# Performance work log

Measured on AMD Instinct MI355X. Metric: run time of the kernel, lower is better.

The kernel has to match this reference:

```python
import jax, jax.numpy as jnp
import numpy as np

N = 50000        # nodes
E = 800000       # edges (before self-loops)
F_IN = 128       # in_features
HID = 128        # hidden_size
HEADS = 4
NEG_SLOPE = 0.2  # PyG GATConv default


def setup_inputs() -> dict:
    key = jax.random.key(0)
    ks = jax.random.split(key, 16)
    def w(k, shape, fan_in):
        return jax.random.normal(k, shape, dtype=jnp.float32) / np.sqrt(fan_in)
    x = jax.random.normal(ks[0], (N, F_IN), dtype=jnp.float32)
    edge_index = jax.random.randint(ks[1], (2, E), 0, N, dtype=jnp.int64)
    return {
        "x": x,
        "edge_index": edge_index,
        # encoder: HEADS independent GATConv(F_IN -> HID, heads=1)
        "enc_W": w(ks[2], (HEADS, F_IN, HID), F_IN),
        "enc_asrc": w(ks[3], (HEADS, HID), HID),
        "enc_adst": w(ks[4], (HEADS, HID), HID),
        "enc_b": jnp.zeros((HEADS, HID), jnp.float32),
        "enc_lin_W": w(ks[5], (HEADS * HID, HID), HEADS * HID),
        "enc_lin_b": jnp.zeros((HID,), jnp.float32),
        # decoder: HEADS independent GATConv(HID -> F_IN, heads=1)
        "dec_W": w(ks[6], (HEADS, HID, F_IN), HID),
        "dec_asrc": w(ks[7], (HEADS, F_IN), F_IN),
        "dec_adst": w(ks[8], (HEADS, F_IN), F_IN),
        "dec_b": jnp.zeros((HEADS, F_IN), jnp.float32),
        "dec_lin_W": w(ks[9], (HEADS * F_IN, F_IN), HEADS * F_IN),
        "dec_lin_b": jnp.zeros((F_IN,), jnp.float32),
    }


def _gat_head(x, src, dst, W, a_src, a_dst, b, n):
    # PyG GATConv, heads=1: h = xW; e = leaky_relu(a_src.h_src + a_dst.h_dst)
    # alpha = segment-softmax over incoming edges of dst; out = scatter-add + b
    h = x @ W                                   # [n, out]
    e = (h @ a_src)[src] + (h @ a_dst)[dst]     # [Etot]
    e = jax.nn.leaky_relu(e, NEG_SLOPE)
    m = jax.ops.segment_max(e, dst, num_segments=n)
    ew = jnp.exp(e - m[dst])
    denom = jax.ops.segment_sum(ew, dst, num_segments=n)
    alpha = ew / denom[dst]                     # self-loops guarantee denom > 0
    out = jax.ops.segment_sum(alpha[:, None] * h[src], dst, num_segments=n)
    return out + b


def _multihead(x, src, dst, Ws, asrc, adst, bs, lin_W, lin_b, n):
    heads = [_gat_head(x, src, dst, Ws[h], asrc[h], adst[h], bs[h], n)
             for h in range(Ws.shape[0])]
    cat = jnp.concatenate(heads, axis=1)        # [n, heads*out]
    return jax.nn.relu(cat @ lin_W + lin_b)


def reference(x, edge_index, enc_W, enc_asrc, enc_adst, enc_b, enc_lin_W,
              enc_lin_b, dec_W, dec_asrc, dec_adst, dec_b, dec_lin_W,
              dec_lin_b):
    n = x.shape[0]
    loop = jnp.arange(n, dtype=edge_index.dtype)
    src = jnp.concatenate([edge_index[0], loop])  # add self-loops (PyG default)
    dst = jnp.concatenate([edge_index[1], loop])
    enc = _multihead(x, src, dst, enc_W, enc_asrc, enc_adst, enc_b,
                     enc_lin_W, enc_lin_b, n)
    dec = _multihead(enc, src, dst, dec_W, dec_asrc, dec_adst, dec_b,
                     dec_lin_W, dec_lin_b, n)
    return dec
```

## Files before the change

### kernel.cpp

```cpp
#include <hip/hip_runtime.h>
#include <hip/hip_fp16.h>
#include <cstdint>
#include <cstddef>


#define FDIM   128
#define HEADS  4
#define HCAT   512

typedef unsigned short u16;
typedef __attribute__((ext_vector_type(4))) float f32x4;
typedef __attribute__((ext_vector_type(8))) short bf16x8;

__device__ __forceinline__ u16 f2b_rne(float f) {
    unsigned u = __float_as_uint(f);
    unsigned r = (u + 0x7FFFu + ((u >> 16) & 1u)) >> 16;
    return (u16)r;
}
__device__ __forceinline__ float b2f(u16 h) {
    return __uint_as_float(((unsigned)h) << 16);
}

__global__ void k_detect(const void* ei, int E, int N, int* flag) {
    if (threadIdx.x == 0 && blockIdx.x == 0) {
        const long long* p = (const long long*)ei;
        int bad = 0;
        int n = E < 64 ? E : 64;
        for (int i = 0; i < n; ++i) {
            long long v = p[i];
            if (v < 0 || v >= (long long)N) bad = 1;
        }
        *flag = bad;
    }
}

__device__ __forceinline__ int edge_at(const void* ei, int is32, long long pos) {
    return is32 ? ((const int*)ei)[pos] : (int)(((const long long*)ei)[pos]);
}

__global__ void k_zero_i32(int* p, int n) {
    int i = blockIdx.x * blockDim.x + threadIdx.x;
    if (i < n) p[i] = 0;
}

__global__ void k_count(const void* ei, const int* flag, int E, int N, int* deg) {
    int e = blockIdx.x * blockDim.x + threadIdx.x;
    int Etot = E + N;
    if (e >= Etot) return;
    int is32 = *flag;
    int dst = (e < E) ? edge_at(ei, is32, (long long)E + e) : (e - E);
    atomicAdd(&deg[dst], 1);
}

#define SCAN_BLOCKS 256
#define SCAN_TPB    256

__global__ __launch_bounds__(SCAN_TPB) void k_scan1(const int* __restrict__ deg,
                                                    int* __restrict__ bsum, int N) {
    __shared__ int sdata[SCAN_TPB];
    int b = blockIdx.x;
    int chunk = (N + SCAN_BLOCKS - 1) / SCAN_BLOCKS;
    int start = b * chunk;
    int end = start + chunk;
    if (start > N) start = N;
    if (end > N) end = N;
    int s = 0;
    for (int i = start + threadIdx.x; i < end; i += SCAN_TPB) s += deg[i];
    sdata[threadIdx.x] = s;
    __syncthreads();
    for (int o = SCAN_TPB / 2; o; o >>= 1) {
        if (threadIdx.x < o) sdata[threadIdx.x] += sdata[threadIdx.x + o];
        __syncthreads();
    }
    if (threadIdx.x == 0) bsum[b] = sdata[0];
}

__global__ __launch_bounds__(SCAN_BLOCKS) void k_scan2(const int* __restrict__ bsum,
                                                       int* __restrict__ bbase,
                                                       int* __restrict__ off_last) {
    __shared__ int sdata[SCAN_BLOCKS];
    int t = threadIdx.x;
    sdata[t] = bsum[t];
    __syncthreads();
    for (int o = 1; o < SCAN_BLOCKS; o <<= 1) {
        int v = (t >= o) ? sdata[t - o] : 0;
        __syncthreads();
        sdata[t] += v;
        __syncthreads();
    }
    bbase[t] = (t == 0) ? 0 : sdata[t - 1];
    if (t == SCAN_BLOCKS - 1) *off_last = sdata[t];
}

__global__ __launch_bounds__(SCAN_TPB) void k_scan3(const int* __restrict__ deg,
                                                    const int* __restrict__ bbase,
                                                    int* __restrict__ off,
                                                    int* __restrict__ cur, int N) {
    __shared__ int sdata[SCAN_TPB];
    int b = blockIdx.x;
    int chunk = (N + SCAN_BLOCKS - 1) / SCAN_BLOCKS;
    int start = b * chunk;
    int end = start + chunk;
    if (start > N) start = N;
    if (end > N) end = N;
    int base = bbase[b];
    for (int i0 = start; i0 < end; i0 += SCAN_TPB) {
        int i = i0 + threadIdx.x;
        int v = (i < end) ? deg[i] : 0;
        sdata[threadIdx.x] = v;
        __syncthreads();
        for (int o = 1; o < SCAN_TPB; o <<= 1) {
            int u = (threadIdx.x >= o) ? sdata[threadIdx.x - o] : 0;
            __syncthreads();
            sdata[threadIdx.x] += u;
            __syncthreads();
        }
        if (i < end) {
            int excl = base + sdata[threadIdx.x] - v;
            off[i] = excl;
            cur[i] = excl;
        }
        base += sdata[SCAN_TPB - 1];
        __syncthreads();
    }
}

__global__ void k_fill(const void* ei, const int* flag, int E, int N, int* cur, int* csr) {
    int e = blockIdx.x * blockDim.x + threadIdx.x;
    int Etot = E + N;
    if (e >= Etot) return;
    int is32 = *flag;
    int src, dst;
    if (e < E) {
        src = edge_at(ei, is32, e);
        dst = edge_at(ei, is32, (long long)E + e);
    } else {
        src = e - E;
        dst = e - E;
    }
    int pos = atomicAdd(&cur[dst], 1);
    csr[pos] = src;
}

__global__ void k_splitw(const float* __restrict__ W, u16* __restrict__ hi,
                         u16* __restrict__ lo, int nblk, int K) {
    int idx = blockIdx.x * blockDim.x + threadIdx.x;
    int total = nblk * K * 128;
    if (idx >= total) return;
    int blk = idx / (K * 128);
    int rem = idx - blk * K * 128;
    int k = rem >> 7, col = rem & 127;
    float v = W[idx];
    u16 h = f2b_rne(v);
    size_t o = (size_t)blk * 128 * K + (size_t)col * K + k;
    hi[o] = h;
    lo[o] = f2b_rne(v - b2f(h));
}

__global__ void k_splitx(const float* __restrict__ X, u16* __restrict__ hi,
                         u16* __restrict__ lo, int n) {
    int i = blockIdx.x * blockDim.x + threadIdx.x;
    if (i >= n) return;
    float v = X[i];
    u16 h = f2b_rne(v);
    hi[i] = h;
    lo[i] = f2b_rne(v - b2f(h));
}

template <int MODE>
__global__ __launch_bounds__(256) void k_gemm_bf(
    const u16* __restrict__ Ahi, const u16* __restrict__ Alo, int lda,
    const u16* __restrict__ Bthi, const u16* __restrict__ Btlo,
    const float* __restrict__ bias,
    const float* __restrict__ asrc, const float* __restrict__ adst,
    float* __restrict__ C, u16* __restrict__ Cb1, u16* __restrict__ Cb2,
    float* __restrict__ ssrc, float* __restrict__ sdst,
    int ldc, int M, int K)
{
    __shared__ alignas(16) char smem[32768];
    const int AHI = 0, ALO = 8192, BHI = 16384, BLO = 24576;
    int tid = threadIdx.x;
    int bm0 = blockIdx.x * 128;
    int yb = blockIdx.y;

    int wid = tid >> 6, lane = tid & 63;
    int wr = wid >> 1, wc = wid & 1;
    int fr = lane & 15, g = lane >> 4;

    f32x4 acc[4][4] = {};

    int arow = tid >> 1, ahalf = tid & 1;
    bool ain = (bm0 + arow) < M;
    const u16* aph = Ahi + (size_t)(bm0 + arow) * lda + ahalf * 16;
    const u16* apl = Alo + (size_t)(bm0 + arow) * lda + ahalf * 16;
    int bcol = tid & 127, bhalf = tid >> 7;
    const u16* bph = Bthi + (size_t)yb * 128 * K + (size_t)bcol * K + bhalf * 16;
    const u16* bpl = Btlo + (size_t)yb * 128 * K + (size_t)bcol * K + bhalf * 16;

    int abase = arow * 64 + ahalf * 32;
    int asw = (arow & 7) << 4;
    int bbase = bcol * 64 + bhalf * 32;
    int bsw = (bcol & 7) << 4;

    for (int k0 = 0; k0 < K; k0 += 32) {
        bf16x8 va0, va1, vl0, vl1;
        if (ain) {
            va0 = *(const bf16x8*)(aph + k0);
            va1 = *(const bf16x8*)(aph + k0 + 8);
            vl0 = *(const bf16x8*)(apl + k0);
            vl1 = *(const bf16x8*)(apl + k0 + 8);
        } else {
            va0 = (bf16x8)0; va1 = (bf16x8)0; vl0 = (bf16x8)0; vl1 = (bf16x8)0;
        }
        bf16x8 vb0 = *(const bf16x8*)(bph + k0);
        bf16x8 vb1 = *(const bf16x8*)(bph + k0 + 8);
        bf16x8 vm0 = *(const bf16x8*)(bpl + k0);
        bf16x8 vm1 = *(const bf16x8*)(bpl + k0 + 8);

        *(bf16x8*)(smem + AHI + ((abase +  0) ^ asw)) = va0;
        *(bf16x8*)(smem + AHI + ((abase + 16) ^ asw)) = va1;
        *(bf16x8*)(smem + ALO + ((abase +  0) ^ asw)) = vl0;
        *(bf16x8*)(smem + ALO + ((abase + 16) ^ asw)) = vl1;
        *(bf16x8*)(smem + BHI + ((bbase +  0) ^ bsw)) = vb0;
        *(bf16x8*)(smem + BHI + ((bbase + 16) ^ bsw)) = vb1;
        *(bf16x8*)(smem + BLO + ((bbase +  0) ^ bsw)) = vm0;
        *(bf16x8*)(smem + BLO + ((bbase + 16) ^ bsw)) = vm1;

        __syncthreads();

        bf16x8 ah[4], al[4], bh[4], bl[4];
#pragma unroll
        for (int mi = 0; mi < 4; ++mi) {
            int r = wr * 64 + mi * 16 + fr;
            int off = (r * 64 + g * 16) ^ ((r & 7) << 4);
            ah[mi] = *(bf16x8*)(smem + AHI + off);
            al[mi] = *(bf16x8*)(smem + ALO + off);
        }
#pragma unroll
        for (int nj = 0; nj < 4; ++nj) {
            int c = wc * 64 + nj * 16 + fr;
            int off = (c * 64 + g * 16) ^ ((c & 7) << 4);
            bh[nj] = *(bf16x8*)(smem + BHI + off);
            bl[nj] = *(bf16x8*)(smem + BLO + off);
        }

#pragma unroll
        for (int mi = 0; mi < 4; ++mi)
#pragma unroll
            for (int nj = 0; nj < 4; ++nj) {
                acc[mi][nj] = __builtin_amdgcn_mfma_f32_16x16x32_bf16(ah[mi], bh[nj], acc[mi][nj], 0, 0, 0);
                acc[mi][nj] = __builtin_amdgcn_mfma_f32_16x16x32_bf16(ah[mi], bl[nj], acc[mi][nj], 0, 0, 0);
                acc[mi][nj] = __builtin_amdgcn_mfma_f32_16x16x32_bf16(al[mi], bh[nj], acc[mi][nj], 0, 0, 0);
            }
        __syncthreads();
    }

#pragma unroll
    for (int mi = 0; mi < 4; ++mi) {
#pragma unroll
        for (int q = 0; q < 4; ++q) {
            int r = bm0 + wr * 64 + mi * 16 + g * 4 + q;
            if (r >= M) continue;
#pragma unroll
            for (int nj = 0; nj < 4; ++nj) {
                int clocal = wc * 64 + nj * 16 + fr;
                float v = acc[mi][nj][q];
                if (MODE == 0) {
                    size_t idx = (size_t)r * ldc + yb * 128 + clocal;
                    __half hv = __float2half(v);
                    Cb1[idx] = *(u16*)&hv;
                } else if (MODE == 1) {
                    v += bias[clocal];
                    v = fmaxf(v, 0.f);
                    size_t idx = (size_t)r * ldc + clocal;
                    u16 h = f2b_rne(v);
                    Cb1[idx] = h;
                    Cb2[idx] = f2b_rne(v - b2f(h));
                } else {
                    v += bias[clocal];
                    v = fmaxf(v, 0.f);
                    C[(size_t)r * ldc + clocal] = v;
                }
            }
        }
    }

    if (MODE == 0) {
        float* sred = (float*)smem;
        float asv[4], adv[4];
        const float* ap = asrc + yb * FDIM;
        const float* dp = adst + yb * FDIM;
#pragma unroll
        for (int nj = 0; nj < 4; ++nj) {
            int c = wc * 64 + nj * 16 + fr;
            asv[nj] = ap[c];
            adv[nj] = dp[c];
        }
#pragma unroll
        for (int mi = 0; mi < 4; ++mi) {
#pragma unroll
            for (int q = 0; q < 4; ++q) {
                float ps = 0.f, pd = 0.f;
#pragma unroll
                for (int nj = 0; nj < 4; ++nj) {
                    ps += acc[mi][nj][q] * asv[nj];
                    pd += acc[mi][nj][q] * adv[nj];
                }
#pragma unroll
                for (int o = 1; o < 16; o <<= 1) {
                    ps += __shfl_xor(ps, o);
                    pd += __shfl_xor(pd, o);
                }
                if (fr == 0) {
                    int row128 = wr * 64 + mi * 16 + g * 4 + q;
                    sred[(row128 * 2 + wc) * 2 + 0] = ps;
                    sred[(row128 * 2 + wc) * 2 + 1] = pd;
                }
            }
        }
        __syncthreads();
        {
            int rg = tid >> 1;
            int which = tid & 1;
            int r = bm0 + rg;
            if (r < M) {
                float v = sred[(rg * 2 + 0) * 2 + which] + sred[(rg * 2 + 1) * 2 + which];
                float* dstp = which ? sdst : ssrc;
                dstp[(size_t)yb * M + r] = v;
            }
        }
    }
}

__global__ __launch_bounds__(64) void k_aggregate(
    const u16* __restrict__ Hb, const int* __restrict__ off,
    const int* __restrict__ csr, const float* __restrict__ ssrc,
    const float* __restrict__ sdst, const float* __restrict__ bvec,
    u16* __restrict__ Ghi, u16* __restrict__ Glo, int N) {
    int n = blockIdx.x;
    int lane = threadIdx.x;
    int o0 = off[n], o1 = off[n + 1];
    int h = lane >> 4;
    int col0 = lane * 8;
    float sdh = sdst[(size_t)h * N + n];
    const float* ssrc_h = ssrc + (size_t)h * N;
    float denom = 0.f;
    float acc[8] = {0.f, 0.f, 0.f, 0.f, 0.f, 0.f, 0.f, 0.f};
    for (int i = o0; i < o1; ++i) {
        int s = csr[i];
        float e = ssrc_h[s] + sdh;
        e = e >= 0.f ? e : 0.2f * e;
        float ew = __expf(e);
        denom += ew;
        uint4 hv = *(const uint4*)&Hb[(size_t)s * HCAT + col0];
        const __half2* hp = (const __half2*)&hv;
#pragma unroll
        for (int j = 0; j < 4; ++j) {
            float2 f = __half22float2(hp[j]);
            acc[2 * j]     += ew * f.x;
            acc[2 * j + 1] += ew * f.y;
        }
    }
    float inv = 1.f / denom;
    u16 hs[8], ls[8];
#pragma unroll
    for (int k = 0; k < 8; ++k) {
        int col = col0 + k;
        float v = acc[k] * inv + bvec[h * FDIM + (col & 127)];
        u16 hbits = f2b_rne(v);
        hs[k] = hbits;
        ls[k] = f2b_rne(v - b2f(hbits));
    }
    *(uint4*)&Ghi[(size_t)n * HCAT + col0] = *(uint4*)hs;
    *(uint4*)&Glo[(size_t)n * HCAT + col0] = *(uint4*)ls;
}

extern "C" void kernel_launch(void* const* d_in, const int* in_sizes, int n_in,
                              void* d_out, int out_size, void* d_ws, size_t ws_size,
                              hipStream_t stream) {
    const float* x = (const float*)d_in[0];
    const void* ei = d_in[1];
    const float* encW = (const float*)d_in[2];
    const float* enc_asrc = (const float*)d_in[3];
    const float* enc_adst = (const float*)d_in[4];
    const float* enc_b = (const float*)d_in[5];
    const float* enc_linW = (const float*)d_in[6];
    const float* enc_linb = (const float*)d_in[7];
    const float* decW = (const float*)d_in[8];
    const float* dec_asrc = (const float*)d_in[9];
    const float* dec_adst = (const float*)d_in[10];
    const float* dec_b = (const float*)d_in[11];
    const float* dec_linW = (const float*)d_in[12];
    const float* dec_linb = (const float*)d_in[13];

    int N = in_sizes[0] / FDIM;
    int E = in_sizes[1] / 2;
    int Etot = E + N;

    char* w = (char*)d_ws;
    size_t o = 0;
    auto alloc = [&](size_t bytes) -> char* {
        char* p = w + o;
        o += (bytes + 255) & ~(size_t)255;
        return p;
    };
    int* flag = (int*)alloc(4);
    int* deg = (int*)alloc((size_t)N * 4);
    int* off = (int*)alloc((size_t)(N + 1) * 4);
    int* cur = (int*)alloc((size_t)N * 4);
    int* csr = (int*)alloc((size_t)Etot * 4);
    int* bsum = (int*)alloc(SCAN_BLOCKS * 4);
    int* bbase = (int*)alloc(SCAN_BLOCKS * 4);
    float* ssrc = (float*)alloc((size_t)HEADS * N * 4);
    float* sdst = (float*)alloc((size_t)HEADS * N * 4);
    u16* Ghi = (u16*)alloc((size_t)N * HCAT * 2);
    u16* Glo = (u16*)alloc((size_t)N * HCAT * 2);
    u16* Hb = (u16*)alloc((size_t)N * HCAT * 2);
    u16* xhi = (u16*)alloc((size_t)N * FDIM * 2);
    u16* xlo = (u16*)alloc((size_t)N * FDIM * 2);
    u16* X2hi = (u16*)alloc((size_t)N * FDIM * 2);
    u16* X2lo = (u16*)alloc((size_t)N * FDIM * 2);
    u16* encWt_h = (u16*)alloc((size_t)HEADS * FDIM * FDIM * 2);
    u16* encWt_l = (u16*)alloc((size_t)HEADS * FDIM * FDIM * 2);
    u16* linWt_h = (u16*)alloc((size_t)HCAT * FDIM * 2);
    u16* linWt_l = (u16*)alloc((size_t)HCAT * FDIM * 2);
    u16* decWt_h = (u16*)alloc((size_t)HEADS * FDIM * FDIM * 2);
    u16* decWt_l = (u16*)alloc((size_t)HEADS * FDIM * FDIM * 2);
    u16* dlinWt_h = (u16*)alloc((size_t)HCAT * FDIM * 2);
    u16* dlinWt_l = (u16*)alloc((size_t)HCAT * FDIM * 2);
    (void)ws_size;

    k_detect<<<1, 64, 0, stream>>>(ei, E, N, flag);
    k_zero_i32<<<(N + 255) / 256, 256, 0, stream>>>(deg, N);
    k_count<<<(Etot + 255) / 256, 256, 0, stream>>>(ei, flag, E, N, deg);
    k_scan1<<<SCAN_BLOCKS, SCAN_TPB, 0, stream>>>(deg, bsum, N);
    k_scan2<<<1, SCAN_BLOCKS, 0, stream>>>(bsum, bbase, off + N);
    k_scan3<<<SCAN_BLOCKS, SCAN_TPB, 0, stream>>>(deg, bbase, off, cur, N);
    k_fill<<<(Etot + 255) / 256, 256, 0, stream>>>(ei, flag, E, N, cur, csr);

    int wtot = HEADS * FDIM * FDIM;
    k_splitw<<<(wtot + 255) / 256, 256, 0, stream>>>(encW, encWt_h, encWt_l, HEADS, FDIM);
    k_splitw<<<(wtot + 255) / 256, 256, 0, stream>>>(enc_linW, linWt_h, linWt_l, 1, HCAT);
    k_splitw<<<(wtot + 255) / 256, 256, 0, stream>>>(decW, decWt_h, decWt_l, HEADS, FDIM);
    k_splitw<<<(wtot + 255) / 256, 256, 0, stream>>>(dec_linW, dlinWt_h, dlinWt_l, 1, HCAT);
    k_splitx<<<(N * FDIM + 255) / 256, 256, 0, stream>>>(x, xhi, xlo, N * FDIM);

    int mblocks = (N + 127) / 128;

    k_gemm_bf<0><<<dim3(mblocks, 4), 256, 0, stream>>>(
        xhi, xlo, FDIM, encWt_h, encWt_l, nullptr, enc_asrc, enc_adst,
        nullptr, Hb, nullptr, ssrc, sdst, HCAT, N, FDIM);
    k_aggregate<<<N, 64, 0, stream>>>(Hb, off, csr, ssrc, sdst, enc_b, Ghi, Glo, N);
    k_gemm_bf<1><<<dim3(mblocks, 1), 256, 0, stream>>>(
        Ghi, Glo, HCAT, linWt_h, linWt_l, enc_linb, nullptr, nullptr,
        nullptr, X2hi, X2lo, nullptr, nullptr, FDIM, N, HCAT);

    k_gemm_bf<0><<<dim3(mblocks, 4), 256, 0, stream>>>(
        X2hi, X2lo, FDIM, decWt_h, decWt_l, nullptr, dec_asrc, dec_adst,
        nullptr, Hb, nullptr, ssrc, sdst, HCAT, N, FDIM);
    k_aggregate<<<N, 64, 0, stream>>>(Hb, off, csr, ssrc, sdst, dec_b, Ghi, Glo, N);
    k_gemm_bf<2><<<dim3(mblocks, 1), 256, 0, stream>>>(
        Ghi, Glo, HCAT, dlinWt_h, dlinWt_l, dec_linb, nullptr, nullptr,
        (float*)d_out, nullptr, nullptr, nullptr, nullptr, FDIM, N, HCAT);
}
```

Before: 594.3 us.

## Switch GEMM activations to single fp16 and unroll aggregate gather by four

Replaces the bf16 hi/lo split of activations with a single fp16 copy, while weights keep an fp16 hi/lo pair. This cuts the MFMA count per tile from three to two and halves activation storage and traffic in the gathers and GEMMs. The aggregate kernel now issues four neighbour loads per iteration to expose more memory parallelism, and reads the CSR bounds with readfirstlane. Accuracy now depends on fp16 range and precision for the activations, which could matter if values grow large.

```diff
diff --git a/kernel.cpp b/kernel.cpp
--- a/kernel.cpp
+++ b/kernel.cpp
@@ -10,15 +10,11 @@
 
 typedef unsigned short u16;
 typedef __attribute__((ext_vector_type(4))) float f32x4;
-typedef __attribute__((ext_vector_type(8))) short bf16x8;
-
-__device__ __forceinline__ u16 f2b_rne(float f) {
-    unsigned u = __float_as_uint(f);
-    unsigned r = (u + 0x7FFFu + ((u >> 16) & 1u)) >> 16;
-    return (u16)r;
-}
-__device__ __forceinline__ float b2f(u16 h) {
-    return __uint_as_float(((unsigned)h) << 16);
+typedef __attribute__((ext_vector_type(8))) _Float16 f16x8;
+
+__device__ __forceinline__ u16 f2h_bits(float f) {
+    _Float16 h = (_Float16)f;
+    return *(u16*)&h;
 }
 
 __global__ void k_detect(const void* ei, int E, int N, int* flag) {
@@ -151,34 +147,31 @@
     int rem = idx - blk * K * 128;
     int k = rem >> 7, col = rem & 127;
     float v = W[idx];
-    u16 h = f2b_rne(v);
+    _Float16 hh = (_Float16)v;
+    _Float16 ll = (_Float16)(v - (float)hh);
     size_t o = (size_t)blk * 128 * K + (size_t)col * K + k;
-    hi[o] = h;
-    lo[o] = f2b_rne(v - b2f(h));
-}
-
-__global__ void k_splitx(const float* __restrict__ X, u16* __restrict__ hi,
-                         u16* __restrict__ lo, int n) {
+    hi[o] = *(u16*)&hh;
+    lo[o] = *(u16*)&ll;
+}
+
+__global__ void k_cvt_f16(const float* __restrict__ X, u16* __restrict__ out, int n) {
     int i = blockIdx.x * blockDim.x + threadIdx.x;
     if (i >= n) return;
-    float v = X[i];
-    u16 h = f2b_rne(v);
-    hi[i] = h;
-    lo[i] = f2b_rne(v - b2f(h));
+    out[i] = f2h_bits(X[i]);
 }
 
 template <int MODE>
-__global__ __launch_bounds__(256) void k_gemm_bf(
-    const u16* __restrict__ Ahi, const u16* __restrict__ Alo, int lda,
+__global__ __launch_bounds__(256) void k_gemm_f16(
+    const u16* __restrict__ A, int lda,
     const u16* __restrict__ Bthi, const u16* __restrict__ Btlo,
     const float* __restrict__ bias,
     const float* __restrict__ asrc, const float* __restrict__ adst,
-    float* __restrict__ C, u16* __restrict__ Cb1, u16* __restrict__ Cb2,
+    float* __restrict__ C, u16* __restrict__ Cb1,
     float* __restrict__ ssrc, float* __restrict__ sdst,
     int ldc, int M, int K)
 {
-    __shared__ alignas(16) char smem[32768];
-    const int AHI = 0, ALO = 8192, BHI = 16384, BLO = 24576;
+    __shared__ alignas(16) char smem[24576];
+    const int ASH = 0, BHI = 8192, BLO = 16384;
     int tid = threadIdx.x;
     int bm0 = blockIdx.x * 128;
     int yb = blockIdx.y;
@@ -191,8 +184,7 @@
 
     int arow = tid >> 1, ahalf = tid & 1;
     bool ain = (bm0 + arow) < M;
-    const u16* aph = Ahi + (size_t)(bm0 + arow) * lda + ahalf * 16;
-    const u16* apl = Alo + (size_t)(bm0 + arow) * lda + ahalf * 16;
+    const u16* aptr = A + (size_t)(bm0 + arow) * lda + ahalf * 16;
     int bcol = tid & 127, bhalf = tid >> 7;
     const u16* bph = Bthi + (size_t)yb * 128 * K + (size_t)bcol * K + bhalf * 16;
     const u16* bpl = Btlo + (size_t)yb * 128 * K + (size_t)bcol * K + bhalf * 16;
@@ -203,54 +195,49 @@
     int bsw = (bcol & 7) << 4;
 
     for (int k0 = 0; k0 < K; k0 += 32) {
-        bf16x8 va0, va1, vl0, vl1;
+        uint4 va0, va1;
         if (ain) {
-            va0 = *(const bf16x8*)(aph + k0);
-            va1 = *(const bf16x8*)(aph + k0 + 8);
-            vl0 = *(const bf16x8*)(apl + k0);
-            vl1 = *(const bf16x8*)(apl + k0 + 8);
+            va0 = *(const uint4*)(aptr + k0);
+            va1 = *(const uint4*)(aptr + k0 + 8);
         } else {
-            va0 = (bf16x8)0; va1 = (bf16x8)0; vl0 = (bf16x8)0; vl1 = (bf16x8)0;
-        }
-        bf16x8 vb0 = *(const bf16x8*)(bph + k0);
-        bf16x8 vb1 = *(const bf16x8*)(bph + k0 + 8);
-        bf16x8 vm0 = *(const bf16x8*)(bpl + k0);
-        bf16x8 vm1 = *(const bf16x8*)(bpl + k0 + 8);
-
-        *(bf16x8*)(smem + AHI + ((abase +  0) ^ asw)) = va0;
-        *(bf16x8*)(smem + AHI + ((abase + 16) ^ asw)) = va1;
-        *(bf16x8*)(smem + ALO + ((abase +  0) ^ asw)) = vl0;
-        *(bf16x8*)(smem + ALO + ((abase + 16) ^ asw)) = vl1;
-        *(bf16x8*)(smem + BHI + ((bbase +  0) ^ bsw)) = vb0;
-        *(bf16x8*)(smem + BHI + ((bbase + 16) ^ bsw)) = vb1;
-        *(bf16x8*)(smem + BLO + ((bbase +  0) ^ bsw)) = vm0;
-        *(bf16x8*)(smem + BLO + ((bbase + 16) ^ bsw)) = vm1;
-
-        __syncthreads();
-
-        bf16x8 ah[4], al[4], bh[4], bl[4];
+            va0 = make_uint4(0, 0, 0, 0);
+            va1 = make_uint4(0, 0, 0, 0);
+        }
+        uint4 vb0 = *(const uint4*)(bph + k0);
+        uint4 vb1 = *(const uint4*)(bph + k0 + 8);
+        uint4 vm0 = *(const uint4*)(bpl + k0);
+        uint4 vm1 = *(const uint4*)(bpl + k0 + 8);
+
+        *(uint4*)(smem + ASH + ((abase +  0) ^ asw)) = va0;
+        *(uint4*)(smem + ASH + ((abase + 16) ^ asw)) = va1;
+        *(uint4*)(smem + BHI + ((bbase +  0) ^ bsw)) = vb0;
+        *(uint4*)(smem + BHI + ((bbase + 16) ^ bsw)) = vb1;
+        *(uint4*)(smem + BLO + ((bbase +  0) ^ bsw)) = vm0;
+        *(uint4*)(smem + BLO + ((bbase + 16) ^ bsw)) = vm1;
+
+        __syncthreads();
+
+        f16x8 af[4], bh[4], bl[4];
 #pragma unroll
         for (int mi = 0; mi < 4; ++mi) {
             int r = wr * 64 + mi * 16 + fr;
             int off = (r * 64 + g * 16) ^ ((r & 7) << 4);
-            ah[mi] = *(bf16x8*)(smem + AHI + off);
-            al[mi] = *(bf16x8*)(smem + ALO + off);
+            af[mi] = *(f16x8*)(smem + ASH + off);
         }
 #pragma unroll
         for (int nj = 0; nj < 4; ++nj) {
             int c = wc * 64 + nj * 16 + fr;
             int off = (c * 64 + g * 16) ^ ((c & 7) << 4);
-            bh[nj] = *(bf16x8*)(smem + BHI + off);
-            bl[nj] = *(bf16x8*)(smem + BLO + off);
+            bh[nj] = *(f16x8*)(smem + BHI + off);
+            bl[nj] = *(f16x8*)(smem + BLO + off);
         }
 
 #pragma unroll
         for (int mi = 0; mi < 4; ++mi)
 #pragma unroll
             for (int nj = 0; nj < 4; ++nj) {
-                acc[mi][nj] = __builtin_amdgcn_mfma_f32_16x16x32_bf16(ah[mi], bh[nj], acc[mi][nj], 0, 0, 0);
-                acc[mi][nj] = __builtin_amdgcn_mfma_f32_16x16x32_bf16(ah[mi], bl[nj], acc[mi][nj], 0, 0, 0);
-                acc[mi][nj] = __builtin_amdgcn_mfma_f32_16x16x32_bf16(al[mi], bh[nj], acc[mi][nj], 0, 0, 0);
+                acc[mi][nj] = __builtin_amdgcn_mfma_f32_16x16x32_f16(af[mi], bh[nj], acc[mi][nj], 0, 0, 0);
+                acc[mi][nj] = __builtin_amdgcn_mfma_f32_16x16x32_f16(af[mi], bl[nj], acc[mi][nj], 0, 0, 0);
             }
         __syncthreads();
     }
@@ -266,16 +253,11 @@
                 int clocal = wc * 64 + nj * 16 + fr;
                 float v = acc[mi][nj][q];
                 if (MODE == 0) {
-                    size_t idx = (size_t)r * ldc + yb * 128 + clocal;
-                    __half hv = __float2half(v);
-                    Cb1[idx] = *(u16*)&hv;
+                    Cb1[(size_t)r * ldc + yb * 128 + clocal] = f2h_bits(v);
                 } else if (MODE == 1) {
                     v += bias[clocal];
                     v = fmaxf(v, 0.f);
-                    size_t idx = (size_t)r * ldc + clocal;
-                    u16 h = f2b_rne(v);
-                    Cb1[idx] = h;
-                    Cb2[idx] = f2b_rne(v - b2f(h));
+                    Cb1[(size_t)r * ldc + clocal] = f2h_bits(v);
                 } else {
                     v += bias[clocal];
                     v = fmaxf(v, 0.f);
@@ -336,43 +318,67 @@
     const u16* __restrict__ Hb, const int* __restrict__ off,
     const int* __restrict__ csr, const float* __restrict__ ssrc,
     const float* __restrict__ sdst, const float* __restrict__ bvec,
-    u16* __restrict__ Ghi, u16* __restrict__ Glo, int N) {
+    u16* __restrict__ Gh, int N) {
     int n = blockIdx.x;
     int lane = threadIdx.x;
-    int o0 = off[n], o1 = off[n + 1];
+    int o0 = __builtin_amdgcn_readfirstlane(off[n]);
+    int o1 = __builtin_amdgcn_readfirstlane(off[n + 1]);
     int h = lane >> 4;
     int col0 = lane * 8;
     float sdh = sdst[(size_t)h * N + n];
     const float* ssrc_h = ssrc + (size_t)h * N;
     float denom = 0.f;
     float acc[8] = {0.f, 0.f, 0.f, 0.f, 0.f, 0.f, 0.f, 0.f};
-    for (int i = o0; i < o1; ++i) {
+
+    auto body = [&](float ew, uint4 hv) {
+        const __half2* hp = (const __half2*)&hv;
+#pragma unroll
+        for (int j = 0; j < 4; ++j) {
+            float2 f = __half22float2(hp[j]);
+            acc[2 * j]     += ew * f.x;
+            acc[2 * j + 1] += ew * f.y;
+        }
+    };
+
+    int i = o0;
+    for (; i + 4 <= o1; i += 4) {
+        int s0 = csr[i + 0], s1 = csr[i + 1], s2 = csr[i + 2], s3 = csr[i + 3];
+        uint4 v0 = *(const uint4*)&Hb[(size_t)s0 * HCAT + col0];
+        uint4 v1 = *(const uint4*)&Hb[(size_t)s1 * HCAT + col0];
+        uint4 v2 = *(const uint4*)&Hb[(size_t)s2 * HCAT + col0];
+        uint4 v3 = *(const uint4*)&Hb[(size_t)s3 * HCAT + col0];
+        float e0 = ssrc_h[s0] + sdh, e1 = ssrc_h[s1] + sdh;
+        float e2 = ssrc_h[s2] + sdh, e3 = ssrc_h[s3] + sdh;
+        e0 = e0 >= 0.f ? e0 : 0.2f * e0;
+        e1 = e1 >= 0.f ? e1 : 0.2f * e1;
+        e2 = e2 >= 0.f ? e2 : 0.2f * e2;
+        e3 = e3 >= 0.f ? e3 : 0.2f * e3;
+        float w0 = __expf(e0), w1 = __expf(e1), w2 = __expf(e2), w3 = __expf(e3);
+        denom += (w0 + w1) + (w2 + w3);
+        body(w0, v0);
+        body(w1, v1);
+        body(w2, v2);
+        body(w3, v3);
+    }
+    for (; i < o1; ++i) {
         int s = csr[i];
+        uint4 v = *(const uint4*)&Hb[(size_t)s * HCAT + col0];
         float e = ssrc_h[s] + sdh;
         e = e >= 0.f ? e : 0.2f * e;
         float ew = __expf(e);
         denom += ew;
-        uint4 hv = *(const uint4*)&Hb[(size_t)s * HCAT + col0];
-        const __half2* hp = (const __half2*)&hv;
-#pragma unroll
-        for (int j = 0; j < 4; ++j) {
-            float2 f = __half22float2(hp[j]);
-            acc[2 * j]     += ew * f.x;
-            acc[2 * j + 1] += ew * f.y;
-        }
-    }
+        body(ew, v);
+    }
+
     float inv = 1.f / denom;
-    u16 hs[8], ls[8];
+    u16 hs[8];
 #pragma unroll
     for (int k = 0; k < 8; ++k) {
         int col = col0 + k;
         float v = acc[k] * inv + bvec[h * FDIM + (col & 127)];
-        u16 hbits = f2b_rne(v);
-        hs[k] = hbits;
-        ls[k] = f2b_rne(v - b2f(hbits));
-    }
-    *(uint4*)&Ghi[(size_t)n * HCAT + col0] = *(uint4*)hs;
-    *(uint4*)&Glo[(size_t)n * HCAT + col0] = *(uint4*)ls;
+        hs[k] = f2h_bits(v);
+    }
+    *(uint4*)&Gh[(size_t)n * HCAT + col0] = *(uint4*)hs;
 }
 
 extern "C" void kernel_launch(void* const* d_in, const int* in_sizes, int n_in,
@@ -413,13 +419,10 @@
     int* bbase = (int*)alloc(SCAN_BLOCKS * 4);
     float* ssrc = (float*)alloc((size_t)HEADS * N * 4);
     float* sdst = (float*)alloc((size_t)HEADS * N * 4);
-    u16* Ghi = (u16*)alloc((size_t)N * HCAT * 2);
-    u16* Glo = (u16*)alloc((size_t)N * HCAT * 2);
+    u16* Gh = (u16*)alloc((size_t)N * HCAT * 2);
     u16* Hb = (u16*)alloc((size_t)N * HCAT * 2);
-    u16* xhi = (u16*)alloc((size_t)N * FDIM * 2);
-    u16* xlo = (u16*)alloc((size_t)N * FDIM * 2);
-    u16* X2hi = (u16*)alloc((size_t)N * FDIM * 2);
-    u16* X2lo = (u16*)alloc((size_t)N * FDIM * 2);
+    u16* xh = (u16*)alloc((size_t)N * FDIM * 2);
+    u16* X2h = (u16*)alloc((size_t)N * FDIM * 2);
     u16* encWt_h = (u16*)alloc((size_t)HEADS * FDIM * FDIM * 2);
     u16* encWt_l = (u16*)alloc((size_t)HEADS * FDIM * FDIM * 2);
     u16* linWt_h = (u16*)alloc((size_t)HCAT * FDIM * 2);
@@ -443,23 +446,23 @@
     k_splitw<<<(wtot + 255) / 256, 256, 0, stream>>>(enc_linW, linWt_h, linWt_l, 1, HCAT);
     k_splitw<<<(wtot + 255) / 256, 256, 0, stream>>>(decW, decWt_h, decWt_l, HEADS, FDIM);
     k_splitw<<<(wtot + 255) / 256, 256, 0, stream>>>(dec_linW, dlinWt_h, dlinWt_l, 1, HCAT);
-    k_splitx<<<(N * FDIM + 255) / 256, 256, 0, stream>>>(x, xhi, xlo, N * FDIM);
+    k_cvt_f16<<<(N * FDIM + 255) / 256, 256, 0, stream>>>(x, xh, N * FDIM);
 
     int mblocks = (N + 127) / 128;
 
-    k_gemm_bf<0><<<dim3(mblocks, 4), 256, 0, stream>>>(
-        xhi, xlo, FDIM, encWt_h, encWt_l, nullptr, enc_asrc, enc_adst,
-        nullptr, Hb, nullptr, ssrc, sdst, HCAT, N, FDIM);
-    k_aggregate<<<N, 64, 0, stream>>>(Hb, off, csr, ssrc, sdst, enc_b, Ghi, Glo, N);
-    k_gemm_bf<1><<<dim3(mblocks, 1), 256, 0, stream>>>(
-        Ghi, Glo, HCAT, linWt_h, linWt_l, enc_linb, nullptr, nullptr,
-        nullptr, X2hi, X2lo, nullptr, nullptr, FDIM, N, HCAT);
-
-    k_gemm_bf<0><<<dim3(mblocks, 4), 256, 0, stream>>>(
-        X2hi, X2lo, FDIM, decWt_h, decWt_l, nullptr, dec_asrc, dec_adst,
-        nullptr, Hb, nullptr, ssrc, sdst, HCAT, N, FDIM);
-    k_aggregate<<<N, 64, 0, stream>>>(Hb, off, csr, ssrc, sdst, dec_b, Ghi, Glo, N);
-    k_gemm_bf<2><<<dim3(mblocks, 1), 256, 0, stream>>>(
-        Ghi, Glo, HCAT, dlinWt_h, dlinWt_l, dec_linb, nullptr, nullptr,
-        (float*)d_out, nullptr, nullptr, nullptr, nullptr, FDIM, N, HCAT);
-}
+    k_gemm_f16<0><<<dim3(mblocks, 4), 256, 0, stream>>>(
+        xh, FDIM, encWt_h, encWt_l, nullptr, enc_asrc, enc_adst,
+        nullptr, Hb, ssrc, sdst, HCAT, N, FDIM);
+    k_aggregate<<<N, 64, 0, stream>>>(Hb, off, csr, ssrc, sdst, enc_b, Gh, N);
+    k_gemm_f16<1><<<dim3(mblocks, 1), 256, 0, stream>>>(
+        Gh, HCAT, linWt_h, linWt_l, enc_linb, nullptr, nullptr,
+        nullptr, X2h, nullptr, nullptr, FDIM, N, HCAT);
+
+    k_gemm_f16<0><<<dim3(mblocks, 4), 256, 0, stream>>>(
+        X2h, FDIM, decWt_h, decWt_l, nullptr, dec_asrc, dec_adst,
+        nullptr, Hb, ssrc, sdst, HCAT, N, FDIM);
+    k_aggregate<<<N, 64, 0, stream>>>(Hb, off, csr, ssrc, sdst, dec_b, Gh, N);
+    k_gemm_f16<2><<<dim3(mblocks, 1), 256, 0, stream>>>(
+        Gh, HCAT, dlinWt_h, dlinWt_l, dec_linb, nullptr, nullptr,
+        (float*)d_out, nullptr, nullptr, nullptr, FDIM, N, HCAT);
+}
```

New measurement: 533.6 us. 1.11x faster.
